# Performance work log

Hardware: AMD Instinct MI355X
Metric: run time of the kernel (lower is better)

The kernel has to match this reference:

```python
import jax, jax.numpy as jnp
import numpy as np

B, T, C, H, N = 2, 1024, 2048, 32, 64  # batch, seq, n_embd==dim_att, heads, head_size
EPS_GN = 64e-5  # torch GroupNorm eps=0.00064


def setup_inputs() -> dict:
    key = jax.random.key(0)
    ks = jax.random.split(key, 40)
    def rn(i, shape, s):
        return jax.random.normal(ks[i], shape, dtype=jnp.float32) * s
    return {
        'x': jax.random.normal(ks[0], (B, T, C), dtype=jnp.float32),
        'shift_state': jnp.zeros((B, C), jnp.float32),
        'wkv_state': jnp.zeros((B, H, N, N), jnp.float32),
        'time_maa_x': rn(1, (1, 1, C), 0.3),
        'time_maa_rg': rn(2, (1, 1, C), 0.3),
        'time_maa_wa': rn(3, (1, 1, C), 0.3),
        'time_maa_k': rn(4, (1, 1, C), 0.3),
        'time_maa_v': rn(5, (1, 1, C), 0.3),
        'time_maa_w1': rn(6, (C, 128), 0.02),   # D_MIX_LORA*4 = 128
        'time_maa_w2': rn(7, (4, 32, C), 0.02),
        'time_decay': rn(8, (1, 1, C), 0.5) - 4.0,
        'time_decay_w1': rn(9, (C, 64), 0.02),
        'time_decay_w2': rn(10, (64, C), 0.02),
        'time_faaaa': rn(11, (1, 1, H, N), 0.02),
        'time_aaaaa': rn(12, (1, 1, C), 0.02),
        'time_aaa_w1': rn(13, (C, 16), 0.02),
        'time_aaa_w2': rn(14, (16, C), 0.02),
        'time_kkk_w1': rn(15, (C, 16), 0.02),
        'time_kkk_w2': rn(16, (16, C), 0.02),
        'gate_w1': rn(17, (C, 128), 0.02),
        'gate_w2': rn(18, (128, C), 0.02),
        'ma_w1': rn(19, (C, 16), 0.02),
        'ma_w2': rn(20, (16, C), 0.02),
        'time_misc_a': rn(21, (1, 1, C), 0.02),
        'mk_w1': rn(22, (C, 16), 0.02),
        'mk_w2': rn(23, (16, C), 0.02),
        'time_misc_k': rn(24, (1, 1, C), 0.02),
        'Wr': rn(25, (C, C), 0.5 / np.sqrt(C)),
        'Wk': rn(26, (C, C), 0.05 / np.sqrt(C)),
        'Wv': rn(27, (C, C), 0.5 / np.sqrt(C)),
        'Wo': rn(28, (C, C), 0.5 / np.sqrt(C)),
        'ln_w': jnp.ones((C,), jnp.float32),
        'ln_b': jnp.zeros((C,), jnp.float32),
    }


def _forward(x, shift_state, wkv_state, time_maa_x, time_maa_rg, time_maa_wa,
             time_maa_k, time_maa_v, time_maa_w1, time_maa_w2, time_decay,
             time_decay_w1, time_decay_w2, time_faaaa, time_aaaaa, time_aaa_w1,
             time_aaa_w2, time_kkk_w1, time_kkk_w2, gate_w1, gate_w2, ma_w1,
             ma_w2, time_misc_a, mk_w1, mk_w2, time_misc_k, Wr, Wk, Wv, Wo,
             ln_w, ln_b):
    # token shift difference
    xx = jnp.concatenate([shift_state[:, None, :], x[:, :-1]], axis=1) - x
    xmx = x + xx * time_maa_x
    m = jnp.tanh(xmx @ time_maa_w1).reshape(B, T, 4, -1)   # [B,T,4,32]
    m = jnp.einsum('btfd,fdc->fbtc', m, time_maa_w2)       # [4,B,T,C]
    mrg, mwa, mkm, mv = m[0], m[1], m[2], m[3]
    xrg = x + xx * (time_maa_rg + mrg)
    xwa = x + xx * (time_maa_wa + mwa)
    xk = x + xx * (time_maa_k + mkm)
    xv = x + xx * (time_maa_v + mv)
    r = xrg @ Wr.T
    w = -jax.nn.softplus(-(time_decay + jnp.tanh(xwa @ time_decay_w1) @ time_decay_w2)) - 0.5
    k = xk @ Wk.T
    v = xv @ Wv.T
    g = jnp.tanh(xrg @ gate_w1) @ gate_w2
    kk = k + jnp.tanh(xk @ time_kkk_w1) @ time_kkk_w2
    kkh = kk.reshape(B, T, H, N)
    nrm = jnp.maximum(jnp.linalg.norm(kkh, axis=-1, keepdims=True), 1e-12)  # F.normalize
    kk = (kkh / nrm).reshape(B, T, C)
    a = jax.nn.sigmoid(time_aaaaa + xwa @ time_aaa_w1 @ time_aaa_w2)
    ma = jax.nn.sigmoid(time_misc_a + xwa @ ma_w1 @ ma_w2)
    k = k * ma + k * a * (1.0 - ma)
    mk = jax.nn.sigmoid(time_misc_k + xk @ mk_w1 @ mk_w2)
    k = k * jnp.exp(jnp.minimum(w * mk, 0.0))  # clamp(w*mk, max=0).exp()

    # RWKV-7 recurrence (fused_recurrent_rwkv7 with a=-kk, b=kk*a_gate):
    #   S_t = diag(exp(w_t)) S_{t-1} + b_t (a_t^T S_{t-1}) + k_t v_t^T,  o_t = S_t^T r_t
    def heads(t):
        return jnp.moveaxis(t.reshape(B, T, H, N), 1, 0)  # [T,B,H,N]
    rs, ksq, vs, ws = heads(r), heads(k), heads(v), heads(w)
    a_s, b_s = heads(-kk), heads(kk * a)

    def step(S, inputs):  # S: [B,H,N_key,N_val]
        r_t, k_t, v_t, w_t, a_t, b_t = inputs
        sa = jnp.einsum('bhk,bhkv->bhv', a_t, S)
        S = S * jnp.exp(w_t)[..., None] + k_t[..., None] * v_t[..., None, :] + b_t[..., None] * sa[..., None, :]
        o = jnp.einsum('bhk,bhkv->bhv', r_t, S)
        return S, o

    S_final, o = jax.lax.scan(step, wkv_state, (rs, ksq, vs, ws, a_s, b_s))
    out = jnp.moveaxis(o, 0, 1).reshape(B, T, C)

    # GroupNorm(n_head groups, eps=64e-5), biased variance per head
    y = out.reshape(B * T, H, N)
    mu = y.mean(-1, keepdims=True)
    var = ((y - mu) ** 2).mean(-1, keepdims=True)
    y = (y - mu) / jnp.sqrt(var + EPS_GN)
    y = y * ln_w.reshape(H, N) + ln_b.reshape(H, N)
    xo = y.reshape(B, T, C)

    rh = r.reshape(B, T, H, N)
    kh = k.reshape(B, T, H, N)
    vh = v.reshape(B, T, H, N)
    xo = xo + ((rh * kh * time_faaaa).sum(-1, keepdims=True) * vh).reshape(B, T, C)
    xo = (xo * g) @ Wo.T
    return xo, x[:, -1], S_final


def reference(x, shift_state, wkv_state, time_maa_x, time_maa_rg, time_maa_wa,
              time_maa_k, time_maa_v, time_maa_w1, time_maa_w2, time_decay,
              time_decay_w1, time_decay_w2, time_faaaa, time_aaaaa, time_aaa_w1,
              time_aaa_w2, time_kkk_w1, time_kkk_w2, gate_w1, gate_w2, ma_w1,
              ma_w2, time_misc_a, mk_w1, mk_w2, time_misc_k, Wr, Wk, Wv, Wo,
              ln_w, ln_b):
    return _forward(x, shift_state, wkv_state, time_maa_x, time_maa_rg, time_maa_wa,
                    time_maa_k, time_maa_v, time_maa_w1, time_maa_w2, time_decay,
                    time_decay_w1, time_decay_w2, time_faaaa, time_aaaaa, time_aaa_w1,
                    time_aaa_w2, time_kkk_w1, time_kkk_w2, gate_w1, gate_w2, ma_w1,
                    ma_w2, time_misc_a, mk_w1, mk_w2, time_misc_k, Wr, Wk, Wv, Wo,
                    ln_w, ln_b)
```

## Files before the change

### kernel.cpp

```cpp
#include <hip/hip_runtime.h>
#include <hip/hip_bf16.h>
#include <math.h>


#define B_ 2
#define T_ 1024
#define C_ 2048
#define H_ 32
#define BT_ (B_*T_)
#define BTC_ ((size_t)BT_*C_)
#define CC_ ((size_t)C_*C_)
#define KS_ 8
#define CH_ 8

typedef __bf16 bf16x8 __attribute__((ext_vector_type(8)));
typedef float f32x4 __attribute__((ext_vector_type(4)));

__device__ __forceinline__ float wave64_sum(float v){
#pragma unroll
  for (int d = 1; d < 64; d <<= 1) v += __shfl_xor(v, d, 64);
  return v;
}

__device__ __forceinline__ float dpp_add_xor1(float x){
  int j = __builtin_amdgcn_mov_dpp(__float_as_int(x), 0xB1, 0xF, 0xF, true);
  return x + __int_as_float(j);
}
__device__ __forceinline__ float dpp_add_xor2(float x){
  int j = __builtin_amdgcn_mov_dpp(__float_as_int(x), 0x4E, 0xF, 0xF, true);
  return x + __int_as_float(j);
}
__device__ __forceinline__ float dpp_add_hmir(float x){
  int j = __builtin_amdgcn_mov_dpp(__float_as_int(x), 0x141, 0xF, 0xF, true);
  return x + __int_as_float(j);
}
__device__ __forceinline__ float dpp_add_mir(float x){
  int j = __builtin_amdgcn_mov_dpp(__float_as_int(x), 0x140, 0xF, 0xF, true);
  return x + __int_as_float(j);
}

__device__ __forceinline__ size_t bhtn_idx(int r, int c){
  return (((size_t)(r >> 10)*H_ + (c >> 6))*T_ + (r & 1023))*64 + (c & 63);
}

__global__ __launch_bounds__(256) void f2bf_kernel(const float* __restrict__ in,
                                                   __hip_bfloat16* __restrict__ out, size_t n){
  size_t i = (size_t)blockIdx.x*256 + threadIdx.x;
  if (i < n) out[i] = __float2bfloat16(in[i]);
}

__global__ __launch_bounds__(256) void shift_kernel(const float* __restrict__ x,
                                                    const float* __restrict__ shift,
                                                    const float* __restrict__ maa_x,
                                                    float* __restrict__ xx, __hip_bfloat16* __restrict__ xmx_h){
  size_t idx = (size_t)blockIdx.x*256 + threadIdx.x;
  int c = (int)(idx % C_);
  size_t bt = idx / C_;
  int t = (int)(bt % T_);
  int b = (int)(bt / T_);
  float xv = x[idx];
  float prev = (t == 0) ? shift[(size_t)b*C_ + c] : x[idx - C_];
  float d = prev - xv;
  xx[idx] = d;
  xmx_h[idx] = __float2bfloat16(xv + d * maa_x[c]);
}

__global__ __launch_bounds__(256) void tp_pack(const float* __restrict__ in, __hip_bfloat16* __restrict__ out,
                                               int Nsrc, int row_off){
  __shared__ float tile[32][33];
  const int t = threadIdx.x;
  const int k0 = blockIdx.x*32, n0 = blockIdx.y*32;
  const int tn = t & 31, tk = t >> 5;
#pragma unroll
  for (int q = 0; q < 4; q++){
    int ki = tk + 8*q;
    float v = (n0 + tn < Nsrc) ? in[(size_t)(k0+ki)*Nsrc + n0 + tn] : 0.f;
    tile[tn][ki] = v;
  }
  __syncthreads();
#pragma unroll
  for (int q = 0; q < 4; q++){
    int no = tk + 8*q;
    if (n0 + no < Nsrc)
      out[(size_t)(row_off + n0 + no)*2048 + k0 + tn] = __float2bfloat16(tile[no][tn]);
  }
}

__global__ __launch_bounds__(256) void gemm_sk(const __hip_bfloat16* __restrict__ Ah,
                                               const __hip_bfloat16* __restrict__ Bh,
                                               float* __restrict__ parts, int K, int KC){
  __shared__ __bf16 As[128*40];
  __shared__ __bf16 Bs[128*40];
  const int tid = threadIdx.x;
  const int bm = blockIdx.x*128;
  const int z = blockIdx.y;
  const int wid = tid >> 6, lane = tid & 63;
  const int wr = (wid >> 1)*64, wc = (wid & 1)*64;
  const int fr = lane & 15, kg = lane >> 4;
  const int srow = tid >> 2, sk = (tid & 3)*8;
  f32x4 acc[4][4] = {};
  const int kend = z*KC + KC;
  for (int kt = z*KC; kt < kend; kt += 32){
    __syncthreads();
    uint4 a0 = *(const uint4*)(Ah + (size_t)(bm+srow)*K + kt + sk);
    uint4 a1 = *(const uint4*)(Ah + (size_t)(bm+srow+64)*K + kt + sk);
    uint4 b0 = *(const uint4*)(Bh + (size_t)(srow)*K + kt + sk);
    uint4 b1 = *(const uint4*)(Bh + (size_t)(srow+64)*K + kt + sk);
    *(uint4*)(As + srow*40 + sk)      = a0;
    *(uint4*)(As + (srow+64)*40 + sk) = a1;
    *(uint4*)(Bs + srow*40 + sk)      = b0;
    *(uint4*)(Bs + (srow+64)*40 + sk) = b1;
    __syncthreads();
    bf16x8 af[4], bfr[4];
#pragma unroll
    for (int i = 0; i < 4; i++){
      af[i]  = *(const bf16x8*)(As + (wr + i*16 + fr)*40 + kg*8);
      bfr[i] = *(const bf16x8*)(Bs + (wc + i*16 + fr)*40 + kg*8);
    }
#pragma unroll
    for (int mi = 0; mi < 4; mi++)
#pragma unroll
      for (int ni = 0; ni < 4; ni++)
        acc[mi][ni] = __builtin_amdgcn_mfma_f32_16x16x32_bf16(af[mi], bfr[ni], acc[mi][ni], 0, 0, 0);
  }
  float* Cc = parts + (size_t)z*BT_*128;
  const int orow0 = bm + wr + kg*4;
  const int ocol0 = wc + fr;
#pragma unroll
  for (int mi = 0; mi < 4; mi++)
#pragma unroll
    for (int ni = 0; ni < 4; ni++)
#pragma unroll
      for (int j = 0; j < 4; j++)
        Cc[(size_t)(orow0 + mi*16 + j)*128 + ocol0 + ni*16] = acc[mi][ni][j];
}

__global__ __launch_bounds__(256) void reduce_sk(const float* __restrict__ parts, float* __restrict__ out,
                                                 int tanh_lo, int tanh_hi){
  size_t idx = (size_t)blockIdx.x*256 + threadIdx.x;
  float s = 0.f;
#pragma unroll
  for (int z = 0; z < KS_; z++) s += parts[(size_t)z*BT_*128 + idx];
  int c = (int)(idx & 127);
  if (c >= tanh_lo && c < tanh_hi) s = tanhf(s);
  out[idx] = s;
}

__global__ __launch_bounds__(256) void mm_sk_g(const float* __restrict__ A, const float* __restrict__ W,
                                               __hip_bfloat16* __restrict__ out, int K){
  const int j = blockIdx.y*256 + threadIdx.x;
  const int i0 = blockIdx.x*8;
  float acc[8] = {0,0,0,0,0,0,0,0};
  for (int k = 0; k < K; k++){
    float wv = W[(size_t)k*C_ + j];
#pragma unroll
    for (int r = 0; r < 8; r++) acc[r] += A[(size_t)(i0+r)*K + k] * wv;
  }
#pragma unroll
  for (int r = 0; r < 8; r++) out[(size_t)(i0+r)*C_ + j] = __float2bfloat16(acc[r]);
}

__global__ __launch_bounds__(256) void mix_kernel(
    const float* __restrict__ m1, const float* __restrict__ w2,
    const float* __restrict__ x, const float* __restrict__ xx,
    const float* __restrict__ maa_rg, const float* __restrict__ maa_wa,
    const float* __restrict__ maa_k, const float* __restrict__ maa_v,
    __hip_bfloat16* __restrict__ xrg_h, __hip_bfloat16* __restrict__ xwa_h,
    __hip_bfloat16* __restrict__ xk_h, __hip_bfloat16* __restrict__ xv_h)
{
  const int j = blockIdx.y*256 + threadIdx.x;
  const int i0 = blockIdx.x*8;
  float acc[4][8] = {};
#pragma unroll
  for (int f = 0; f < 4; f++){
    for (int d = 0; d < 32; d++){
      float wv = w2[((size_t)f*32 + d)*C_ + j];
#pragma unroll
      for (int r = 0; r < 8; r++)
        acc[f][r] += m1[(size_t)(i0+r)*128 + f*32 + d] * wv;
    }
  }
  float mrg_ = maa_rg[j], mwa_ = maa_wa[j], mk_ = maa_k[j], mv_ = maa_v[j];
#pragma unroll
  for (int r = 0; r < 8; r++){
    size_t idx = (size_t)(i0+r)*C_ + j;
    float xval = x[idx], xxv = xx[idx];
    xrg_h[idx] = __float2bfloat16(xval + xxv*(mrg_ + acc[0][r]));
    xwa_h[idx] = __float2bfloat16(xval + xxv*(mwa_ + acc[1][r]));
    xk_h[idx]  = __float2bfloat16(xval + xxv*(mk_  + acc[2][r]));
    xv_h[idx]  = __float2bfloat16(xval + xxv*(mv_  + acc[3][r]));
  }
}

__global__ __launch_bounds__(256) void gemm_bt(const __hip_bfloat16* __restrict__ Ah,
                                               const __hip_bfloat16* __restrict__ Bh,
                                               float* __restrict__ Cc, int M, int Nn, int K){
  __shared__ __bf16 As[128*40];
  __shared__ __bf16 Bs[128*40];
  const int tid = threadIdx.x;
  const int bm = blockIdx.x*128, bn = blockIdx.y*128;
  const int wid = tid >> 6, lane = tid & 63;
  const int wr = (wid >> 1)*64, wc = (wid & 1)*64;
  const int fr = lane & 15, kg = lane >> 4;
  const int srow = tid >> 2, sk = (tid & 3)*8;
  f32x4 acc[4][4] = {};
  for (int kt = 0; kt < K; kt += 32){
    __syncthreads();
    uint4 a0 = *(const uint4*)(Ah + (size_t)(bm+srow)*K + kt + sk);
    uint4 a1 = *(const uint4*)(Ah + (size_t)(bm+srow+64)*K + kt + sk);
    uint4 b0 = *(const uint4*)(Bh + (size_t)(bn+srow)*K + kt + sk);
    uint4 b1 = *(const uint4*)(Bh + (size_t)(bn+srow+64)*K + kt + sk);
    *(uint4*)(As + srow*40 + sk)      = a0;
    *(uint4*)(As + (srow+64)*40 + sk) = a1;
    *(uint4*)(Bs + srow*40 + sk)      = b0;
    *(uint4*)(Bs + (srow+64)*40 + sk) = b1;
    __syncthreads();
    bf16x8 af[4], bfr[4];
#pragma unroll
    for (int i = 0; i < 4; i++){
      af[i]  = *(const bf16x8*)(As + (wr + i*16 + fr)*40 + kg*8);
      bfr[i] = *(const bf16x8*)(Bs + (wc + i*16 + fr)*40 + kg*8);
    }
#pragma unroll
    for (int mi = 0; mi < 4; mi++)
#pragma unroll
      for (int ni = 0; ni < 4; ni++)
        acc[mi][ni] = __builtin_amdgcn_mfma_f32_16x16x32_bf16(af[mi], bfr[ni], acc[mi][ni], 0, 0, 0);
  }
  const int orow0 = bm + wr + kg*4;
  const int ocol0 = bn + wc + fr;
#pragma unroll
  for (int mi = 0; mi < 4; mi++)
#pragma unroll
    for (int ni = 0; ni < 4; ni++)
#pragma unroll
      for (int j = 0; j < 4; j++)
        Cc[(size_t)(orow0 + mi*16 + j)*Nn + ocol0 + ni*16] = acc[mi][ni][j];
}

__global__ __launch_bounds__(256) void gemm_bt_T(const __hip_bfloat16* __restrict__ Ah,
                                                 const __hip_bfloat16* __restrict__ Bh,
                                                 float* __restrict__ Cc, int K){
  __shared__ __bf16 As[128*40];
  __shared__ __bf16 Bs[128*40];
  const int tid = threadIdx.x;
  const int bm = blockIdx.x*128, bn = blockIdx.y*128;
  const int wid = tid >> 6, lane = tid & 63;
  const int wr = (wid >> 1)*64, wc = (wid & 1)*64;
  const int fr = lane & 15, kg = lane >> 4;
  const int srow = tid >> 2, sk = (tid & 3)*8;
  f32x4 acc[4][4] = {};
  for (int kt = 0; kt < K; kt += 32){
    __syncthreads();
    uint4 a0 = *(const uint4*)(Ah + (size_t)(bm+srow)*K + kt + sk);
    uint4 a1 = *(const uint4*)(Ah + (size_t)(bm+srow+64)*K + kt + sk);
    uint4 b0 = *(const uint4*)(Bh + (size_t)(bn+srow)*K + kt + sk);
    uint4 b1 = *(const uint4*)(Bh + (size_t)(bn+srow+64)*K + kt + sk);
    *(uint4*)(As + srow*40 + sk)      = a0;
    *(uint4*)(As + (srow+64)*40 + sk) = a1;
    *(uint4*)(Bs + srow*40 + sk)      = b0;
    *(uint4*)(Bs + (srow+64)*40 + sk) = b1;
    __syncthreads();
    bf16x8 af[4], bfr[4];
#pragma unroll
    for (int i = 0; i < 4; i++){
      af[i]  = *(const bf16x8*)(As + (wr + i*16 + fr)*40 + kg*8);
      bfr[i] = *(const bf16x8*)(Bs + (wc + i*16 + fr)*40 + kg*8);
    }
#pragma unroll
    for (int mi = 0; mi < 4; mi++)
#pragma unroll
      for (int ni = 0; ni < 4; ni++)
        acc[mi][ni] = __builtin_amdgcn_mfma_f32_16x16x32_bf16(af[mi], bfr[ni], acc[mi][ni], 0, 0, 0);
  }
  const int r0 = bm + wr + kg*4;
  const int c0 = bn + wc + fr;
#pragma unroll
  for (int mi = 0; mi < 4; mi++)
#pragma unroll
    for (int ni = 0; ni < 4; ni++)
#pragma unroll
      for (int j = 0; j < 4; j++)
        Cc[bhtn_idx(r0 + mi*16 + j, c0 + ni*16)] = acc[mi][ni][j];
}

__global__ __launch_bounds__(256) void lora2_kernel(
    const float* __restrict__ wa1, const float* __restrict__ k1c,
    const float* __restrict__ dw2, const float* __restrict__ aw2, const float* __restrict__ maw2,
    const float* __restrict__ mkw2, const float* __restrict__ kkw2,
    const float* __restrict__ td, const float* __restrict__ aaaaa,
    const float* __restrict__ misc_a, const float* __restrict__ misc_k,
    float* __restrict__ k0, float* __restrict__ a_out,
    float* __restrict__ ew_out, float* __restrict__ kk0_out)
{
  const int j = blockIdx.y*256 + threadIdx.x;
  const int i0 = blockIdx.x*8;
  float accW[8] = {}, accA[8] = {}, accMA[8] = {}, accMK[8] = {}, accKK[8] = {};
  for (int k = 0; k < 64; k++){
    float wv = dw2[(size_t)k*C_ + j];
#pragma unroll
    for (int r = 0; r < 8; r++) accW[r] += wa1[(size_t)(i0+r)*128 + k] * wv;
  }
  for (int k = 0; k < 16; k++){
    float w_a  = aw2[(size_t)k*C_ + j];
    float w_ma = maw2[(size_t)k*C_ + j];
    float w_mk = mkw2[(size_t)k*C_ + j];
    float w_kk = kkw2[(size_t)k*C_ + j];
#pragma unroll
    for (int r = 0; r < 8; r++){
      accA[r]  += wa1[(size_t)(i0+r)*128 + 64 + k] * w_a;
      accMA[r] += wa1[(size_t)(i0+r)*128 + 80 + k] * w_ma;
      accKK[r] += k1c[(size_t)(i0+r)*128 + k] * w_kk;
      accMK[r] += k1c[(size_t)(i0+r)*128 + 16 + k] * w_mk;
    }
  }
  float tdv = td[j], aav = aaaaa[j], mav = misc_a[j], mkv = misc_k[j];
#pragma unroll
  for (int r = 0; r < 8; r++){
    size_t idx = bhtn_idx(i0+r, j);
    float u  = tdv + accW[r];
    float w  = -log1pf(expf(-u)) - 0.5f;
    float a  = 1.f/(1.f + expf(-(aav + accA[r])));
    float ma = 1.f/(1.f + expf(-(mav + accMA[r])));
    float mk = 1.f/(1.f + expf(-(mkv + accMK[r])));
    float kv = k0[idx];
    kk0_out[idx] = kv + accKK[r];
    float kn = kv * (ma + a*(1.f - ma)) * expf(fminf(w*mk, 0.f));
    k0[idx] = kn;
    a_out[idx] = a;
    ew_out[idx] = expf(w);
  }
}

__global__ __launch_bounds__(256) void kknorm_kernel(float* __restrict__ kk0, float* __restrict__ a_bs){
  const size_t grp = (size_t)blockIdx.x*4 + (threadIdx.x >> 6);
  const int lane = threadIdx.x & 63;
  const size_t idx = grp*64 + lane;
  float kv = kk0[idx];
  float ss = wave64_sum(kv*kv);
  float nrm = fmaxf(sqrtf(ss), 1e-12f);
  float kkn = kv / nrm;
  kk0[idx] = kkn;
  a_bs[idx] = kkn * a_bs[idx];
}

__device__ __forceinline__ void gload_lds16(const float* g, float* l){
  __builtin_amdgcn_global_load_lds((const __attribute__((address_space(1))) void*)g,
                                   (__attribute__((address_space(3))) void*)l, 16, 0, 0);
}

__global__ __launch_bounds__(64, 1) void rec_kernel(
    const float* __restrict__ rr, const float* __restrict__ kx,
    const float* __restrict__ vx, const float* __restrict__ ew,
    const float* __restrict__ kkv, const float* __restrict__ bsv,
    const float* __restrict__ s0, float* __restrict__ o, float* __restrict__ sT)
{
  __shared__ __align__(16) float lds[2][6][CH_*64];
  const int g = blockIdx.x;
  const int bh = g & 63;
  const int vg = g >> 6;
  const int b = bh >> 5, h = bh & 31;
  const int lane = threadIdx.x;
  const int kq = lane & 15;
  const int cf = lane >> 4;
  const int k0 = kq*4;
  const int v = vg*4 + cf;

  float S0, S1, S2, S3;
  {
    const float* p = s0 + ((size_t)bh*64 + k0)*64 + v;
    S0 = p[0]; S1 = p[64]; S2 = p[128]; S3 = p[192];
  }

  const size_t sb = (size_t)bh*T_*64;
  const float* g0 = kkv + sb;
  const float* g1 = ew  + sb;
  const float* g2 = kx  + sb;
  const float* g3 = bsv + sb;
  const float* g4 = rr  + sb;
  const float* g5 = vx  + sb;
  float* ob = o + (size_t)b*T_*C_ + h*64 + v;

#define STAGE(c, buf) do{ \
    const size_t co_ = (size_t)(c)*(CH_*64) + lane*4; \
    _Pragma("unroll") \
    for (int j_ = 0; j_ < 2; j_++){ \
      gload_lds16(g0 + co_ + j_*256, &lds[buf][0][j_*256]); \
      gload_lds16(g1 + co_ + j_*256, &lds[buf][1][j_*256]); \
      gload_lds16(g2 + co_ + j_*256, &lds[buf][2][j_*256]); \
      gload_lds16(g3 + co_ + j_*256, &lds[buf][3][j_*256]); \
      gload_lds16(g4 + co_ + j_*256, &lds[buf][4][j_*256]); \
      gload_lds16(g5 + co_ + j_*256, &lds[buf][5][j_*256]); \
    } }while(0)

  STAGE(0, 0);
  const int NCH = T_/CH_;
  for (int c = 0; c < NCH; c++){
    const int cn = (c+1 < NCH) ? c+1 : c;
    STAGE(cn, (c+1)&1);
    __builtin_amdgcn_s_waitcnt(0x0F7C);
    __builtin_amdgcn_sched_barrier(0);
    const int buf = c & 1;
#pragma unroll
    for (int s = 0; s < CH_; s++){
      const int so = s*64 + k0;
      const float4 A  = *(const float4*)(&lds[buf][0][so]);
      const float4 E  = *(const float4*)(&lds[buf][1][so]);
      const float4 Kk = *(const float4*)(&lds[buf][2][so]);
      const float4 Bv = *(const float4*)(&lds[buf][3][so]);
      const float4 R  = *(const float4*)(&lds[buf][4][so]);
      const float vt  = lds[buf][5][s*64 + v];
      float p = (A.x*S0 + A.y*S1) + (A.z*S2 + A.w*S3);
      p = dpp_add_xor1(p);
      p = dpp_add_xor2(p);
      p = dpp_add_hmir(p);
      p = dpp_add_mir(p);
      const float sa = -p;
      S0 = S0*E.x + Kk.x*vt + Bv.x*sa;
      S1 = S1*E.y + Kk.y*vt + Bv.y*sa;
      S2 = S2*E.z + Kk.z*vt + Bv.z*sa;
      S3 = S3*E.w + Kk.w*vt + Bv.w*sa;
      float op = (R.x*S0 + R.y*S1) + (R.z*S2 + R.w*S3);
      op = dpp_add_xor1(op);
      op = dpp_add_xor2(op);
      op = dpp_add_hmir(op);
      op = dpp_add_mir(op);
      if (kq == 0) ob[(size_t)(c*CH_ + s)*C_] = op;
    }
  }
#undef STAGE
  float* pT = sT + ((size_t)bh*64 + k0)*64 + v;
  pT[0] = S0; pT[64] = S1; pT[128] = S2; pT[192] = S3;
}

__global__ __launch_bounds__(256) void post_kernel(
    const float* __restrict__ o, const float* __restrict__ r, const float* __restrict__ k,
    const float* __restrict__ v, const __hip_bfloat16* __restrict__ g,
    const float* __restrict__ lnw, const float* __restrict__ lnb,
    const float* __restrict__ faaaa, __hip_bfloat16* __restrict__ z_h)
{
  const size_t grp = (size_t)blockIdx.x*4 + (threadIdx.x >> 6);
  const int lane = threadIdx.x & 63;
  const int h = (int)(grp & (H_-1));
  const int bt = (int)(grp >> 5);
  const size_t idx  = grp*64 + lane;
  const size_t idx2 = (((size_t)(bt >> 10)*H_ + h)*T_ + (bt & 1023))*64 + lane;
  const int ci = h*64 + lane;
  float y = o[idx];
  float mu = wave64_sum(y) * (1.f/64.f);
  float d = y - mu;
  float var = wave64_sum(d*d) * (1.f/64.f);
  float yn = d * rsqrtf(var + 64e-5f) * lnw[ci] + lnb[ci];
  float s = wave64_sum(r[idx2]*k[idx2]*faaaa[ci]);
  float xo = yn + s*v[idx2];
  z_h[idx] = __float2bfloat16(xo * __bfloat162float(g[idx]));
}

__global__ __launch_bounds__(256) void lastx_kernel(const float* __restrict__ x, float* __restrict__ out1){
  int idx = blockIdx.x*256 + threadIdx.x;
  int b = idx / C_, c = idx % C_;
  out1[idx] = x[((size_t)b*T_ + (T_-1))*C_ + c];
}

extern "C" void kernel_launch(void* const* d_in, const int* in_sizes, int n_in,
                              void* d_out, int out_size, void* d_ws, size_t ws_size,
                              hipStream_t stream){
  (void)in_sizes; (void)n_in; (void)out_size;
  const float* x      = (const float*)d_in[0];
  const float* shift  = (const float*)d_in[1];
  const float* wkv0   = (const float*)d_in[2];
  const float* maa_x  = (const float*)d_in[3];
  const float* maa_rg = (const float*)d_in[4];
  const float* maa_wa = (const float*)d_in[5];
  const float* maa_k  = (const float*)d_in[6];
  const float* maa_v  = (const float*)d_in[7];
  const float* maa_w1 = (const float*)d_in[8];
  const float* maa_w2 = (const float*)d_in[9];
  const float* tdecay = (const float*)d_in[10];
  const float* dw1    = (const float*)d_in[11];
  const float* dw2    = (const float*)d_in[12];
  const float* faaaa  = (const float*)d_in[13];
  const float* aaaaa  = (const float*)d_in[14];
  const float* aw1    = (const float*)d_in[15];
  const float* aw2    = (const float*)d_in[16];
  const float* kkw1   = (const float*)d_in[17];
  const float* kkw2   = (const float*)d_in[18];
  const float* gw1    = (const float*)d_in[19];
  const float* gw2    = (const float*)d_in[20];
  const float* maw1   = (const float*)d_in[21];
  const float* maw2   = (const float*)d_in[22];
  const float* misc_a = (const float*)d_in[23];
  const float* mkw1   = (const float*)d_in[24];
  const float* mkw2   = (const float*)d_in[25];
  const float* misc_k = (const float*)d_in[26];
  const float* Wr     = (const float*)d_in[27];
  const float* Wk     = (const float*)d_in[28];
  const float* Wv     = (const float*)d_in[29];
  const float* Wo     = (const float*)d_in[30];
  const float* lnw    = (const float*)d_in[31];
  const float* lnb    = (const float*)d_in[32];

  float* out0 = (float*)d_out;
  float* out1 = out0 + BTC_;
  float* outS = out1 + (size_t)B_*C_;

  const size_t NEEDED = (6*BTC_ + (size_t)3*BT_*128)*4 + 5*CC_*2 + (size_t)4*128*2048*2;
  if (ws_size < NEEDED) return;

  float* ws = (float*)d_ws;
  float* rbuf  = ws;
  float* kbuf  = ws + 1*BTC_;
  float* vbuf  = ws + 2*BTC_;
  float* abuf  = ws + 3*BTC_;
  float* ewbuf = ws + 4*BTC_;
  float* kkbuf = ws + 5*BTC_;
  float* xx    = abuf;
  float* wa1   = ws + 6*BTC_;
  float* g1f   = wa1 + (size_t)BT_*128;
  float* k1c   = g1f + (size_t)BT_*128;
  float* parts = rbuf;
  float* m1f   = vbuf;
  __hip_bfloat16* hb = (__hip_bfloat16*)(k1c + (size_t)BT_*128);
  __hip_bfloat16* xrg_h = hb;
  __hip_bfloat16* xwa_h = hb + 1*CC_;
  __hip_bfloat16* xk_h  = hb + 2*CC_;
  __hip_bfloat16* xv_h  = hb + 3*CC_;
  __hip_bfloat16* Wb    = hb + 4*CC_;
  __hip_bfloat16* WtB   = hb + 5*CC_;
  __hip_bfloat16* Wt_m  = WtB;
  __hip_bfloat16* Wt_wa = WtB + (size_t)128*2048;
  __hip_bfloat16* Wt_g  = WtB + (size_t)2*128*2048;
  __hip_bfloat16* Wt_k  = WtB + (size_t)3*128*2048;
  __hip_bfloat16* xmx_h = xv_h;
  __hip_bfloat16* g_h   = xwa_h;
  __hip_bfloat16* z_h   = xv_h;
  __hip_bfloat16* Wk_h  = (__hip_bfloat16*)ewbuf;
  __hip_bfloat16* Wv_h  = (__hip_bfloat16*)kkbuf;

  dim3 blk(256);
  const int KC = C_/KS_;

  hipMemsetAsync(WtB, 0, (size_t)4*128*2048*2, stream);
  tp_pack<<<dim3(64,4), blk, 0, stream>>>(maa_w1, Wt_m, 128, 0);
  tp_pack<<<dim3(64,2), blk, 0, stream>>>(dw1,  Wt_wa, 64, 0);
  tp_pack<<<dim3(64,1), blk, 0, stream>>>(aw1,  Wt_wa, 16, 64);
  tp_pack<<<dim3(64,1), blk, 0, stream>>>(maw1, Wt_wa, 16, 80);
  tp_pack<<<dim3(64,4), blk, 0, stream>>>(gw1,  Wt_g, 128, 0);
  tp_pack<<<dim3(64,1), blk, 0, stream>>>(kkw1, Wt_k, 16, 0);
  tp_pack<<<dim3(64,1), blk, 0, stream>>>(mkw1, Wt_k, 16, 16);

  shift_kernel<<<(int)(BTC_/256), blk, 0, stream>>>(x, shift, maa_x, xx, xmx_h);

  gemm_sk<<<dim3(BT_/128, KS_), blk, 0, stream>>>(xmx_h, Wt_m, parts, C_, KC);
  reduce_sk<<<BT_*128/256, blk, 0, stream>>>(parts, m1f, 0, 128);

  mix_kernel<<<dim3(BT_/8, C_/256), blk, 0, stream>>>(m1f, maa_w2, x, xx, maa_rg, maa_wa, maa_k, maa_v,
                                                      xrg_h, xwa_h, xk_h, xv_h);
  gemm_sk<<<dim3(BT_/128, KS_), blk, 0, stream>>>(xwa_h, Wt_wa, parts, C_, KC);
  reduce_sk<<<BT_*128/256, blk, 0, stream>>>(parts, wa1, 0, 64);
  gemm_sk<<<dim3(BT_/128, KS_), blk, 0, stream>>>(xrg_h, Wt_g, parts, C_, KC);
  reduce_sk<<<BT_*128/256, blk, 0, stream>>>(parts, g1f, 0, 128);
  gemm_sk<<<dim3(BT_/128, KS_), blk, 0, stream>>>(xk_h, Wt_k, parts, C_, KC);
  reduce_sk<<<BT_*128/256, blk, 0, stream>>>(parts, k1c, 0, 16);

  mm_sk_g<<<dim3(BT_/8, C_/256), blk, 0, stream>>>(g1f, gw2, g_h, 128);

  f2bf_kernel<<<(int)(CC_/256), blk, 0, stream>>>(Wr, Wb, CC_);
  f2bf_kernel<<<(int)(CC_/256), blk, 0, stream>>>(Wk, Wk_h, CC_);
  f2bf_kernel<<<(int)(CC_/256), blk, 0, stream>>>(Wv, Wv_h, CC_);
  gemm_bt_T<<<dim3(BT_/128, C_/128), blk, 0, stream>>>(xrg_h, Wb,   rbuf, C_);
  gemm_bt_T<<<dim3(BT_/128, C_/128), blk, 0, stream>>>(xk_h,  Wk_h, kbuf, C_);
  gemm_bt_T<<<dim3(BT_/128, C_/128), blk, 0, stream>>>(xv_h,  Wv_h, vbuf, C_);

  lora2_kernel<<<dim3(BT_/8, C_/256), blk, 0, stream>>>(wa1, k1c,
                                                        dw2, aw2, maw2, mkw2, kkw2,
                                                        tdecay, aaaaa, misc_a, misc_k,
                                                        kbuf, abuf, ewbuf, kkbuf);
  kknorm_kernel<<<BT_*H_/4, blk, 0, stream>>>(kkbuf, abuf);

  rec_kernel<<<1024, dim3(64), 0, stream>>>(rbuf, kbuf, vbuf, ewbuf, kkbuf, abuf, wkv0, out0, outS);

  post_kernel<<<BT_*H_/4, blk, 0, stream>>>(out0, rbuf, kbuf, vbuf, g_h, lnw, lnb, faaaa, z_h);
  f2bf_kernel<<<(int)(CC_/256), blk, 0, stream>>>(Wo, Wb, CC_);
  gemm_bt<<<dim3(BT_/128, C_/128), blk, 0, stream>>>(z_h, Wb, out0, BT_, C_, C_);
  lastx_kernel<<<(B_*C_)/256, blk, 0, stream>>>(x, out1);
}
```

Baseline: 870.4 us.

## Split recurrence state across more waves with 2 keys per lane

The WKV recurrence kernel now gives each lane 2 state elements instead of 4, with 32 lanes covering the key dimension and 2 value columns per wave. The grid doubles to 2048 wavefronts. A cross-half ds_bpermute step is added to the DPP reduction. The chunk size drops to 4 timesteps so the staging issues one LDS load per array, and the waitcnt is adjusted to match. The aim is to shorten the serial per-step dependency chain and put more waves in flight. In exchange there is extra reduction latency and twice the redundant loads of the shared k/w/a/r vectors.

```diff
diff --git a/kernel.cpp b/kernel.cpp
--- a/kernel.cpp
+++ b/kernel.cpp
@@ -11,7 +11,7 @@
 #define BTC_ ((size_t)BT_*C_)
 #define CC_ ((size_t)C_*C_)
 #define KS_ 8
-#define CH_ 8
+#define CH_ 4
 
 typedef __bf16 bf16x8 __attribute__((ext_vector_type(8)));
 typedef float f32x4 __attribute__((ext_vector_type(4)));
@@ -37,6 +37,15 @@
 __device__ __forceinline__ float dpp_add_mir(float x){
   int j = __builtin_amdgcn_mov_dpp(__float_as_int(x), 0x140, 0xF, 0xF, true);
   return x + __int_as_float(j);
+}
+
+__device__ __forceinline__ float red32(float x, int xaddr){
+  x = dpp_add_xor1(x);
+  x = dpp_add_xor2(x);
+  x = dpp_add_hmir(x);
+  x = dpp_add_mir(x);
+  x += __int_as_float(__builtin_amdgcn_ds_bpermute(xaddr, __float_as_int(x)));
+  return x;
 }
 
 __device__ __forceinline__ size_t bhtn_idx(int r, int c){
@@ -349,7 +358,7 @@
                                    (__attribute__((address_space(3))) void*)l, 16, 0, 0);
 }
 
-__global__ __launch_bounds__(64, 1) void rec_kernel(
+__global__ __launch_bounds__(64, 2) void rec_kernel(
     const float* __restrict__ rr, const float* __restrict__ kx,
     const float* __restrict__ vx, const float* __restrict__ ew,
     const float* __restrict__ kkv, const float* __restrict__ bsv,
@@ -361,15 +370,16 @@
   const int vg = g >> 6;
   const int b = bh >> 5, h = bh & 31;
   const int lane = threadIdx.x;
-  const int kq = lane & 15;
-  const int cf = lane >> 4;
-  const int k0 = kq*4;
-  const int v = vg*4 + cf;
-
-  float S0, S1, S2, S3;
+  const int cf = (lane >> 4) & 1;
+  const int kq = (lane & 15) + ((lane & 32) >> 1);
+  const int k0 = kq*2;
+  const int v = vg*2 + cf;
+  const int xaddr = (lane ^ 32) << 2;
+
+  float S0, S1;
   {
     const float* p = s0 + ((size_t)bh*64 + k0)*64 + v;
-    S0 = p[0]; S1 = p[64]; S2 = p[128]; S3 = p[192];
+    S0 = p[0]; S1 = p[64];
   }
 
   const size_t sb = (size_t)bh*T_*64;
@@ -383,54 +393,44 @@
 
 #define STAGE(c, buf) do{ \
     const size_t co_ = (size_t)(c)*(CH_*64) + lane*4; \
-    _Pragma("unroll") \
-    for (int j_ = 0; j_ < 2; j_++){ \
-      gload_lds16(g0 + co_ + j_*256, &lds[buf][0][j_*256]); \
-      gload_lds16(g1 + co_ + j_*256, &lds[buf][1][j_*256]); \
-      gload_lds16(g2 + co_ + j_*256, &lds[buf][2][j_*256]); \
-      gload_lds16(g3 + co_ + j_*256, &lds[buf][3][j_*256]); \
-      gload_lds16(g4 + co_ + j_*256, &lds[buf][4][j_*256]); \
-      gload_lds16(g5 + co_ + j_*256, &lds[buf][5][j_*256]); \
-    } }while(0)
+    gload_lds16(g0 + co_, &lds[buf][0][0]); \
+    gload_lds16(g1 + co_, &lds[buf][1][0]); \
+    gload_lds16(g2 + co_, &lds[buf][2][0]); \
+    gload_lds16(g3 + co_, &lds[buf][3][0]); \
+    gload_lds16(g4 + co_, &lds[buf][4][0]); \
+    gload_lds16(g5 + co_, &lds[buf][5][0]); \
+  }while(0)
 
   STAGE(0, 0);
   const int NCH = T_/CH_;
   for (int c = 0; c < NCH; c++){
     const int cn = (c+1 < NCH) ? c+1 : c;
     STAGE(cn, (c+1)&1);
-    __builtin_amdgcn_s_waitcnt(0x0F7C);
+    __builtin_amdgcn_s_waitcnt(0x0F76);
     __builtin_amdgcn_sched_barrier(0);
     const int buf = c & 1;
 #pragma unroll
     for (int s = 0; s < CH_; s++){
       const int so = s*64 + k0;
-      const float4 A  = *(const float4*)(&lds[buf][0][so]);
-      const float4 E  = *(const float4*)(&lds[buf][1][so]);
-      const float4 Kk = *(const float4*)(&lds[buf][2][so]);
-      const float4 Bv = *(const float4*)(&lds[buf][3][so]);
-      const float4 R  = *(const float4*)(&lds[buf][4][so]);
+      const float2 A  = *(const float2*)(&lds[buf][0][so]);
+      const float2 E  = *(const float2*)(&lds[buf][1][so]);
+      const float2 Kk = *(const float2*)(&lds[buf][2][so]);
+      const float2 Bv = *(const float2*)(&lds[buf][3][so]);
+      const float2 R  = *(const float2*)(&lds[buf][4][so]);
       const float vt  = lds[buf][5][s*64 + v];
-      float p = (A.x*S0 + A.y*S1) + (A.z*S2 + A.w*S3);
-      p = dpp_add_xor1(p);
-      p = dpp_add_xor2(p);
-      p = dpp_add_hmir(p);
-      p = dpp_add_mir(p);
-      const float sa = -p;
-      S0 = S0*E.x + Kk.x*vt + Bv.x*sa;
-      S1 = S1*E.y + Kk.y*vt + Bv.y*sa;
-      S2 = S2*E.z + Kk.z*vt + Bv.z*sa;
-      S3 = S3*E.w + Kk.w*vt + Bv.w*sa;
-      float op = (R.x*S0 + R.y*S1) + (R.z*S2 + R.w*S3);
-      op = dpp_add_xor1(op);
-      op = dpp_add_xor2(op);
-      op = dpp_add_hmir(op);
-      op = dpp_add_mir(op);
-      if (kq == 0) ob[(size_t)(c*CH_ + s)*C_] = op;
+      float p = A.x*S0 + A.y*S1;
+      p = red32(p, xaddr);
+      S0 = S0*E.x + Kk.x*vt - Bv.x*p;
+      S1 = S1*E.y + Kk.y*vt - Bv.y*p;
+      float op = R.x*S0 + R.y*S1;
+      op = red32(op, xaddr);
+      if ((lane & 0x2F) == 0)
+        ob[(size_t)(c*CH_ + s)*C_] = op;
     }
   }
 #undef STAGE
   float* pT = sT + ((size_t)bh*64 + k0)*64 + v;
-  pT[0] = S0; pT[64] = S1; pT[128] = S2; pT[192] = S3;
+  pT[0] = S0; pT[64] = S1;
 }
 
 __global__ __launch_bounds__(256) void post_kernel(
@@ -578,7 +578,7 @@
                                                         kbuf, abuf, ewbuf, kkbuf);
   kknorm_kernel<<<BT_*H_/4, blk, 0, stream>>>(kkbuf, abuf);
 
-  rec_kernel<<<1024, dim3(64), 0, stream>>>(rbuf, kbuf, vbuf, ewbuf, kkbuf, abuf, wkv0, out0, outS);
+  rec_kernel<<<2048, dim3(64), 0, stream>>>(rbuf, kbuf, vbuf, ewbuf, kkbuf, abuf, wkv0, out0, outS);
 
   post_kernel<<<BT_*H_/4, blk, 0, stream>>>(out0, rbuf, kbuf, vbuf, g_h, lnw, lnb, faaaa, z_h);
   f2bf_kernel<<<(int)(CC_/256), blk, 0, stream>>>(Wo, Wb, CC_);
```

Result: slower. 966.6 us (+11.1%).
